# Kernel optimization log

Measured on AMD Instinct MI355X. Metric: run time of the kernel, lower is better.

## Reference

```python
import jax, jax.numpy as jnp
import numpy as np

B, H, W, CP, CI = 2, 256, 256, 256, 256
IN, OUT = CP + CI, CP          # in_dims=512, out_dims=256
WS, NH, L = 8, 8, 2            # window, heads, num blocks
N = WS * WS                    # tokens per window
HD = OUT // NH                 # head dim = 32
SCALE = HD ** -0.5

def _rel_pos_index():
    c = np.stack(np.meshgrid(np.arange(WS), np.arange(WS), indexing='ij')).reshape(2, -1)
    r = (c[:, :, None] - c[:, None, :]).transpose(1, 2, 0)
    r[..., 0] += WS - 1
    r[..., 1] += WS - 1
    r[..., 0] *= 2 * WS - 1
    return r.sum(-1)  # [N, N] int

REL_IDX = _rel_pos_index()

def _attn_mask(shift):
    img = np.zeros((H, W))
    cnt = 0
    for hs in (slice(0, -WS), slice(-WS, -shift), slice(-shift, None)):
        for ws_ in (slice(0, -WS), slice(-WS, -shift), slice(-shift, None)):
            img[hs, ws_] = cnt
            cnt += 1
    m = img.reshape(H // WS, WS, W // WS, WS).transpose(0, 2, 1, 3).reshape(-1, N)
    d = m[:, None, :] - m[:, :, None]
    return jnp.asarray(np.where(d != 0, -100.0, 0.0).astype(np.float32))  # [nW, N, N]

MASK = _attn_mask(WS // 2)

def _ln(x, g, b, eps=1e-5):
    m = x.mean(-1, keepdims=True)
    v = ((x - m) ** 2).mean(-1, keepdims=True)
    return (x - m) * jax.lax.rsqrt(v + eps) * g + b

def _win_attn(x, qkv_w, qkv_b, rpb_t, proj_w, proj_b, shift):
    # x: [B,H,W,C]
    if shift > 0:
        x = jnp.roll(x, (-shift, -shift), axis=(1, 2))
    nW = (H // WS) * (W // WS)
    xw = x.reshape(B, H // WS, WS, W // WS, WS, OUT).transpose(0, 1, 3, 2, 4, 5).reshape(B, nW, N, OUT)
    qkv = (xw @ qkv_w.T + qkv_b).reshape(B, nW, N, 3, NH, HD)
    q, k, v = qkv[..., 0, :, :], qkv[..., 1, :, :], qkv[..., 2, :, :]  # [B,nW,N,NH,HD]
    attn = jnp.einsum('bwqhd,bwkhd->bwhqk', q * SCALE, k)  # [B,nW,NH,N,N]
    bias = rpb_t[REL_IDX.reshape(-1)].reshape(N, N, NH).transpose(2, 0, 1)  # [NH,N,N]
    attn = attn + bias
    if shift > 0:
        attn = attn + MASK[None, :, None, :, :]
    attn = jax.nn.softmax(attn, axis=-1)
    out = jnp.einsum('bwhqk,bwkhd->bwqhd', attn, v).reshape(B, nW, N, OUT)
    out = out @ proj_w.T + proj_b
    out = out.reshape(B, H // WS, W // WS, WS, WS, OUT).transpose(0, 1, 3, 2, 4, 5).reshape(B, H, W, OUT)
    if shift > 0:
        out = jnp.roll(out, (shift, shift), axis=(1, 2))
    return out

def setup_inputs() -> dict:
    key = jax.random.key(0)
    ks = jax.random.split(key, 12)
    s = 0.02
    p = {}
    p['pcd'] = jax.random.normal(ks[0], (B, H, W, CP), jnp.float32)
    p['img'] = jax.random.normal(ks[1], (B, H, W, CI), jnp.float32)
    p['rd_w1'] = jax.random.normal(ks[2], (4 * IN, IN), jnp.float32) * s
    p['rd_b1'] = jnp.zeros((4 * IN,), jnp.float32)
    p['rd_lng'] = jnp.ones((4 * IN,), jnp.float32)
    p['rd_lnb'] = jnp.zeros((4 * IN,), jnp.float32)
    p['rd_w2'] = jax.random.normal(ks[3], (OUT, 4 * IN), jnp.float32) * s
    p['rd_b2'] = jnp.zeros((OUT,), jnp.float32)
    p['n1g'] = jnp.ones((L, OUT), jnp.float32)
    p['n1b'] = jnp.zeros((L, OUT), jnp.float32)
    p['qkv_w'] = jax.random.normal(ks[4], (L, 3 * OUT, OUT), jnp.float32) * s
    p['qkv_b'] = jnp.zeros((L, 3 * OUT), jnp.float32)
    p['rpb'] = jax.random.normal(ks[5], (L, (2 * WS - 1) ** 2, NH), jnp.float32) * s
    p['proj_w'] = jax.random.normal(ks[6], (L, OUT, OUT), jnp.float32) * s
    p['proj_b'] = jnp.zeros((L, OUT), jnp.float32)
    p['n2g'] = jnp.ones((L, OUT), jnp.float32)
    p['n2b'] = jnp.zeros((L, OUT), jnp.float32)
    p['mlp_w1'] = jax.random.normal(ks[7], (L, 4 * OUT, OUT), jnp.float32) * s
    p['mlp_b1'] = jnp.zeros((L, 4 * OUT), jnp.float32)
    p['mlp_w2'] = jax.random.normal(ks[8], (L, OUT, 4 * OUT), jnp.float32) * s
    p['mlp_b2'] = jnp.zeros((L, OUT), jnp.float32)
    return p

def reference(pcd, img, rd_w1, rd_b1, rd_lng, rd_lnb, rd_w2, rd_b2,
              n1g, n1b, qkv_w, qkv_b, rpb, proj_w, proj_b,
              n2g, n2b, mlp_w1, mlp_b1, mlp_w2, mlp_b2):
    # reduce_dim: Linear -> LeakyReLU(0.01) -> LayerNorm -> Linear
    x = jnp.concatenate([pcd, img], axis=3)
    x = x @ rd_w1.T + rd_b1
    x = jnp.where(x > 0, x, 0.01 * x)
    x = _ln(x, rd_lng, rd_lnb)
    x = x @ rd_w2.T + rd_b2
    # two SwinTransformerBlocks (shift 0, then WS//2)
    for i in range(L):
        shift = 0 if i % 2 == 0 else WS // 2
        x = x + _win_attn(_ln(x, n1g[i], n1b[i]), qkv_w[i], qkv_b[i], rpb[i], proj_w[i], proj_b[i], shift)
        h = _ln(x, n2g[i], n2b[i])
        h = jax.nn.gelu(h @ mlp_w1[i].T + mlp_b1[i], approximate=False)
        x = x + h @ mlp_w2[i].T + mlp_b2[i]
    return x + pcd
```

## Files before the change

kernel.cpp:

```cpp
#include <hip/hip_runtime.h>
#include <math.h>

typedef __attribute__((ext_vector_type(4))) float f32x4v;
typedef __attribute__((ext_vector_type(8))) __bf16 bf16x8v;
typedef __attribute__((ext_vector_type(2))) uint u32x2v;
typedef __attribute__((ext_vector_type(4))) uint u32x4v;

#define SCALE 0.17677669529663687f
#define TOK 131072
#define MCHUNK 32768
#define T32 ((long)TOK * 32)
#define C32 ((long)MCHUNK * 32)

__device__ __forceinline__ ushort f2bf(float v){
  const __bf16 b = (__bf16)v;
  return __builtin_bit_cast(ushort, b);
}
__device__ __forceinline__ float bflo(uint u){ return __uint_as_float(u << 16); }
__device__ __forceinline__ float bfhi(uint u){ return __uint_as_float(u & 0xffff0000u); }
__device__ __forceinline__ float bf2f(ushort u){ return __uint_as_float((uint)u << 16); }

__global__ __launch_bounds__(256) void cvtw_k(const float* __restrict__ src,
    ushort* __restrict__ dst, int K, long m32, int n4){
  const int i = blockIdx.x * 256 + threadIdx.x;
  if (i >= n4) return;
  const int flat = i * 4;
  const int r = flat / K, k = flat % K;
  float4 v = ((const float4*)src)[i];
  ushort4 o = { f2bf(v.x), f2bf(v.y), f2bf(v.z), f2bf(v.w) };
  *(ushort4*)(dst + (long)(k >> 5) * m32 + (long)r * 32 + (k & 31)) = o;
}

__global__ __launch_bounds__(64) void cvtwg_k(const float* __restrict__ src,
    const float* __restrict__ gma, const float* __restrict__ bta,
    ushort* __restrict__ dst, float* __restrict__ c1, float* __restrict__ c2,
    int K, long m32){
  const int n = blockIdx.x, lane = threadIdx.x;
  const float* sp = src + (long)n * K;
  float s1 = 0.f, s2 = 0.f;
  for (int k = lane * 4; k < K; k += 256){
    float4 wv = *(const float4*)(sp + k);
    float4 gv = *(const float4*)(gma + k);
    float4 bv = *(const float4*)(bta + k);
    s1 += wv.x * gv.x + wv.y * gv.y + wv.z * gv.z + wv.w * gv.w;
    s2 += wv.x * bv.x + wv.y * bv.y + wv.z * bv.z + wv.w * bv.w;
    ushort4 o = { f2bf(wv.x * gv.x), f2bf(wv.y * gv.y), f2bf(wv.z * gv.z), f2bf(wv.w * gv.w) };
    *(ushort4*)(dst + (long)(k >> 5) * m32 + (long)n * 32 + (k & 31)) = o;
  }
  #pragma unroll
  for (int o = 1; o < 64; o <<= 1){ s1 += __shfl_xor(s1, o); s2 += __shfl_xor(s2, o); }
  if (lane == 0){ c1[n] = s1; c2[n] = s2; }
}

__global__ __launch_bounds__(256) void concat_k(const float* __restrict__ pcd,
    const float* __restrict__ img, ushort* __restrict__ A0){
  const long gid = (long)blockIdx.x * 256 + threadIdx.x;
  const long t = gid >> 7;
  const int c4 = (int)(gid & 127) * 4;
  const float* src = (c4 < 256) ? (pcd + t * 256 + c4) : (img + t * 256 + (c4 - 256));
  float4 v = *(const float4*)src;
  ushort4 o = { f2bf(v.x), f2bf(v.y), f2bf(v.z), f2bf(v.w) };
  const long chunk = t >> 15, tc = t & 32767;
  ushort* dst = A0 + chunk * 16777216 + (long)(c4 >> 5) * C32 + tc * 32 + (c4 & 31);
  __builtin_nontemporal_store(*(u32x2v*)&o, (u32x2v*)dst);
}

__global__ __launch_bounds__(256) void statsred_k(const float* __restrict__ pb,
    float* __restrict__ stats){
  const int row = blockIdx.x * 256 + threadIdx.x;
  const float2* p = (const float2*)(pb + (long)row * 64);
  float s = 0.f, q = 0.f;
  #pragma unroll
  for (int i = 0; i < 32; ++i){ const float2 v = p[i]; s += v.x; q += v.y; }
  const float mean = s * (1.f / 2048.f);
  const float var = q * (1.f / 2048.f) - mean * mean;
  stats[row * 2] = mean;
  stats[row * 2 + 1] = rsqrtf(var + 1e-5f);
}

__global__ __launch_bounds__(256) void stats256b_k(const ushort* __restrict__ xb,
    float* __restrict__ stats){
  const int lane = threadIdx.x & 63, wd = threadIdx.x >> 6;
  const long row = (long)blockIdx.x * 4 + wd;
  uint2 u = *(const uint2*)(xb + (long)(lane >> 3) * T32 + row * 32 + (lane & 7) * 4);
  float a = bflo(u.x), b2 = bfhi(u.x), c = bflo(u.y), d = bfhi(u.y);
  float s = a + b2 + c + d;
  float q = a * a + b2 * b2 + c * c + d * d;
  #pragma unroll
  for (int o = 1; o < 64; o <<= 1){ s += __shfl_xor(s, o); q += __shfl_xor(q, o); }
  if (lane == 0){
    float mean = s * (1.f / 256.f);
    float var = q * (1.f / 256.f) - mean * mean;
    stats[row * 2] = mean;
    stats[row * 2 + 1] = rsqrtf(var + 1e-5f);
  }
}

template<int ACT, int OUTT, int RES, bool LNEPI, int MINB>
__global__ __launch_bounds__(256, MINB) void gemm_k(
    const ushort* __restrict__ A, const ushort* __restrict__ W,
    const float* __restrict__ bias,
    float* __restrict__ outf, ushort* __restrict__ outb,
    const ushort* __restrict__ res, const float* __restrict__ pcdp,
    const float* __restrict__ stats, const float* __restrict__ c1v,
    const float* __restrict__ c2v, int N, int K, int gx,
    long aM32, long wM32, long oM32, int mOff, float* __restrict__ ost)
{
  __shared__ ushort SH[16384];
  const int tid = threadIdx.x;
  const int lane = tid & 63, w = tid >> 6;
  const int nwg = gridDim.x;
  const int xcd = blockIdx.x & 7;
  const int idx = blockIdx.x >> 3;
  const int mPerX = nwg / (8 * gx);
  const int sg = idx / (8 * gx);
  const int u  = idx - sg * (8 * gx);
  const int nT = u >> 3;
  const int ml = u & 7;
  const int mBase = (xcd * mPerX + sg * 8 + ml) * 128;
  const int nBase = nT * 128;
  const int fr = lane & 15, grp = lane >> 4;
  const int wr = w >> 1, wc = w & 1;

  f32x4v acc[4][4];
  #pragma unroll
  for (int i = 0; i < 4; ++i)
    #pragma unroll
    for (int j = 0; j < 4; ++j) acc[i][j] = (f32x4v){0.f, 0.f, 0.f, 0.f};

  const long aBase = (long)(mBase + w * 32) * 32 + lane * 8;
  const long wBase = (long)(nBase + w * 32) * 32 + lane * 8;
  ushort* Ad0 = &SH[w * 1024 + lane * 8];
  ushort* Bd0 = &SH[4096 + w * 1024 + lane * 8];
  ushort* Ad1 = &SH[8192 + w * 1024 + lane * 8];
  ushort* Bd1 = &SH[12288 + w * 1024 + lane * 8];

  const int NT = K >> 5;

#define MFMASTEP(ao, bo) do { \
    bf16x8v af[4], bv[4]; \
    _Pragma("unroll") \
    for (int i = 0; i < 4; ++i) \
      af[i] = *(const bf16x8v*)&SH[(ao) + (wr * 64 + i * 16 + fr) * 32 + grp * 8]; \
    _Pragma("unroll") \
    for (int j = 0; j < 4; ++j) \
      bv[j] = *(const bf16x8v*)&SH[(bo) + (wc * 64 + j * 16 + fr) * 32 + grp * 8]; \
    _Pragma("unroll") \
    for (int i = 0; i < 4; ++i) \
      _Pragma("unroll") \
      for (int j = 0; j < 4; ++j) \
        acc[i][j] = __builtin_amdgcn_mfma_f32_16x16x32_bf16(af[i], bv[j], acc[i][j], 0, 0, 0); \
  } while (0)

  {
    uint4 x0 = *(const uint4*)(A + aBase);
    uint4 x1 = *(const uint4*)(A + aBase + 512);
    uint4 y0 = *(const uint4*)(W + wBase);
    uint4 y1 = *(const uint4*)(W + wBase + 512);
    *(uint4*)Ad0 = x0; *(uint4*)(Ad0 + 512) = x1;
    *(uint4*)Bd0 = y0; *(uint4*)(Bd0 + 512) = y1;
  }
  uint4 pa0 = *(const uint4*)(A + aBase + aM32);
  uint4 pa1 = *(const uint4*)(A + aBase + aM32 + 512);
  uint4 pb0 = *(const uint4*)(W + wBase + wM32);
  uint4 pb1 = *(const uint4*)(W + wBase + wM32 + 512);
  uint4 qa0 = *(const uint4*)(A + aBase + 2 * aM32);
  uint4 qa1 = *(const uint4*)(A + aBase + 2 * aM32 + 512);
  uint4 qb0 = *(const uint4*)(W + wBase + 2 * wM32);
  uint4 qb1 = *(const uint4*)(W + wBase + 2 * wM32 + 512);
  __syncthreads();

  for (int t = 0; t < NT; t += 2){
    MFMASTEP(0, 4096);
    *(uint4*)Ad1 = pa0; *(uint4*)(Ad1 + 512) = pa1;
    *(uint4*)Bd1 = pb0; *(uint4*)(Bd1 + 512) = pb1;
    if (t + 3 < NT){
      const long ao = aBase + (long)(t + 3) * aM32;
      const long wo = wBase + (long)(t + 3) * wM32;
      pa0 = *(const uint4*)(A + ao);
      pa1 = *(const uint4*)(A + ao + 512);
      pb0 = *(const uint4*)(W + wo);
      pb1 = *(const uint4*)(W + wo + 512);
    }
    __syncthreads();
    MFMASTEP(8192, 12288);
    if (t + 2 < NT){
      *(uint4*)Ad0 = qa0; *(uint4*)(Ad0 + 512) = qa1;
      *(uint4*)Bd0 = qb0; *(uint4*)(Bd0 + 512) = qb1;
      if (t + 4 < NT){
        const long ao = aBase + (long)(t + 4) * aM32;
        const long wo = wBase + (long)(t + 4) * wM32;
        qa0 = *(const uint4*)(A + ao);
        qa1 = *(const uint4*)(A + ao + 512);
        qb0 = *(const uint4*)(W + wo);
        qb1 = *(const uint4*)(W + wo + 512);
      }
    }
    __syncthreads();
  }
#undef MFMASTEP

  float muv[16], rsv[16];
  if (LNEPI){
    #pragma unroll
    for (int i = 0; i < 4; ++i)
      #pragma unroll
      for (int rr = 0; rr < 4; ++rr){
        const int m = mBase + wr * 64 + i * 16 + grp * 4 + rr;
        muv[i * 4 + rr] = stats[m * 2];
        rsv[i * 4 + rr] = stats[m * 2 + 1];
      }
  }
  float rsum[16], rsq[16];
  if (ost){
    #pragma unroll
    for (int t2 = 0; t2 < 16; ++t2){ rsum[t2] = 0.f; rsq[t2] = 0.f; }
  }
  #pragma unroll
  for (int j = 0; j < 4; ++j){
    const int n = nBase + wc * 64 + j * 16 + fr;
    const float bn = bias[n];
    float c1n = 0.f, c2n = 0.f;
    if (LNEPI){ c1n = c1v[n]; c2n = c2v[n]; }
    #pragma unroll
    for (int i = 0; i < 4; ++i){
      #pragma unroll
      for (int rr = 0; rr < 4; ++rr){
        const long m = mBase + wr * 64 + i * 16 + grp * 4 + rr;
        float v = acc[i][j][rr];
        if (LNEPI) v = rsv[i * 4 + rr] * v - muv[i * 4 + rr] * rsv[i * 4 + rr] * c1n + c2n;
        v += bn;
        if (ACT == 1) v = v > 0.f ? v : 0.01f * v;
        if (ACT == 2){
          const float u2 = v * (0.7978845608f + 0.0356774081f * v * v);
          const float t2 = 1.f - 2.f * __builtin_amdgcn_rcpf(__expf(2.f * u2) + 1.f);
          v = 0.5f * v * (1.f + t2);
        }
        if (RES >= 1)
          v += bf2f(res[(long)(n >> 5) * T32 + (mOff + m) * 32 + (n & 31)]);
        if (RES == 2) v += pcdp[(mOff + m) * N + n];
        acc[i][j][rr] = v;
        if (ost){ rsum[i * 4 + rr] += v; rsq[i * 4 + rr] += v * v; }
        if (OUTT == 0) __builtin_nontemporal_store(v, &outf[(mOff + m) * N + n]);
      }
    }
  }
  if (ost){
    const int nT4 = nT * 4 + wc * 2;
    #pragma unroll
    for (int t2 = 0; t2 < 16; ++t2){
      float s = rsum[t2], q = rsq[t2];
      #pragma unroll
      for (int o = 1; o < 16; o <<= 1){ s += __shfl_xor(s, o); q += __shfl_xor(q, o); }
      if (fr == 0){
        const long m = mBase + wr * 64 + (t2 >> 2) * 16 + grp * 4 + (t2 & 3);
        ost[m * 64 + nT4]     = s;
        ost[m * 64 + nT4 + 1] = q;
      }
    }
  }
  if (OUTT == 1){
    ushort* eb = &SH[0];
    __syncthreads();
    #pragma unroll
    for (int p = 0; p < 2; ++p){
      if (wr == p){
        #pragma unroll
        for (int i = 0; i < 4; ++i)
          #pragma unroll
          for (int rr = 0; rr < 4; ++rr){
            const int rl = i * 16 + grp * 4 + rr;
            #pragma unroll
            for (int j = 0; j < 4; ++j)
              eb[rl * 128 + wc * 64 + j * 16 + fr] = f2bf(acc[i][j][rr]);
          }
      }
      __syncthreads();
      #pragma unroll
      for (int it = 0; it < 4; ++it){
        const int c = it * 256 + tid;
        const int row = c >> 4, cg = c & 15;
        const u32x4v val = *(const u32x4v*)&eb[row * 128 + cg * 8];
        ushort* dst = outb + (long)((nBase >> 5) + (cg >> 2)) * oM32
                    + (long)(mOff + mBase + p * 64 + row) * 32 + (cg & 3) * 8;
        __builtin_nontemporal_store(val, (u32x4v*)dst);
      }
      __syncthreads();
    }
  }
}

template<int SHIFT>
__global__ __launch_bounds__(256, 2) void attn_k(const ushort* __restrict__ qkv,
    const float* __restrict__ rpb, ushort* __restrict__ outp)
{
  __shared__ ushort Vt[4][2312];
  __shared__ ushort Pl[4][4616];
  __shared__ float bias_s[4][226];
  __shared__ int code_s[64];
  const int tid = threadIdx.x;
  const int lane = tid & 63, wid = tid >> 6;
  const int hg = blockIdx.x & 1;
  const int bw = blockIdx.x >> 1;
  const int b = bw >> 10, widx = bw & 1023;
  const int wh = widx >> 5, ww = widx & 31;
  const int head = hg * 4 + wid;
  const int fr = lane & 15, grp = lane >> 4;

  for (int i = lane; i < 225; i += 64) bias_s[wid][i] = rpb[i * 8 + head];
  if (SHIFT > 0 && tid < 64){
    const int hh = wh * 8 + (tid >> 3), wwp = ww * 8 + (tid & 7);
    const int rh = (hh < 248) ? 0 : ((hh < 256 - SHIFT) ? 1 : 2);
    const int rw = (wwp < 248) ? 0 : ((wwp < 256 - SHIFT) ? 1 : 2);
    code_s[tid] = rh * 3 + rw;
  }
  #pragma unroll
  for (int it = 0; it < 4; ++it){
    const int c = it * 256 + tid;
    const int row = c >> 4, part = c & 15;
    const int hc = part >> 2, dc = part & 3;
    const int hs = (wh * 8 + (row >> 3) + SHIFT) & 255;
    const int wsm = (ww * 8 + (row & 7) + SHIFT) & 255;
    const long tk = ((long)b * 256 + hs) * 256 + wsm;
    const uint4 vu = *(const uint4*)(qkv + (long)(16 + hg * 4 + hc) * T32 + tk * 32 + dc * 8);
    const ushort* ve = (const ushort*)&vu;
    #pragma unroll
    for (int e = 0; e < 8; ++e)
      Vt[hc][(dc * 8 + e) * 72 + row] = ve[e];
  }
  long tokr[4];
  #pragma unroll
  for (int j = 0; j < 4; ++j){
    const int n = j * 16 + fr;
    const int hs = (wh * 8 + (n >> 3) + SHIFT) & 255;
    const int wsm = (ww * 8 + (n & 7) + SHIFT) & 255;
    tokr[j] = ((long)b * 256 + hs) * 256 + wsm;
  }
  bf16x8v kf[4];
  #pragma unroll
  for (int j = 0; j < 4; ++j)
    kf[j] = *(const bf16x8v*)(qkv + (long)(8 + head) * T32 + tokr[j] * 32 + grp * 8);
  __syncthreads();

  float invs[4][4];
  #pragma unroll
  for (int qi = 0; qi < 4; ++qi){
    const bf16x8v qf = *(const bf16x8v*)(qkv + (long)head * T32 + tokr[qi] * 32 + grp * 8);
    f32x4v sc[4];
    #pragma unroll
    for (int ci = 0; ci < 4; ++ci)
      sc[ci] = __builtin_amdgcn_mfma_f32_16x16x32_bf16(qf, kf[ci],
          (f32x4v){0.f, 0.f, 0.f, 0.f}, 0, 0, 0);
    #pragma unroll
    for (int rr = 0; rr < 4; ++rr){
      const int q = qi * 16 + grp * 4 + rr;
      const int thq = q >> 3, twq = q & 7;
      int codeq = 0;
      if (SHIFT > 0){
        const int hq = wh * 8 + thq, wq = ww * 8 + twq;
        const int rh = (hq < 248) ? 0 : ((hq < 256 - SHIFT) ? 1 : 2);
        const int rw = (wq < 248) ? 0 : ((wq < 256 - SHIFT) ? 1 : 2);
        codeq = rh * 3 + rw;
      }
      const int lbase = (thq + 7 - (fr >> 3)) * 15 + (twq + 7 - (fr & 7));
      float sum = 0.f;
      #pragma unroll
      for (int ci = 0; ci < 4; ++ci){
        float s = sc[ci][rr] * SCALE + bias_s[wid][lbase - ci * 30];
        if (SHIFT > 0 && codeq != code_s[ci * 16 + fr]) s -= 100.f;
        const float p = __expf(s);
        sum += p;
        Pl[wid][q * 72 + ci * 16 + fr] = f2bf(p);
      }
      sum += __shfl_xor(sum, 1);
      sum += __shfl_xor(sum, 2);
      sum += __shfl_xor(sum, 4);
      sum += __shfl_xor(sum, 8);
      invs[qi][rr] = __builtin_amdgcn_rcpf(sum);
    }
  }
  f32x4v o[4][2];
  #pragma unroll
  for (int qi = 0; qi < 4; ++qi)
    #pragma unroll
    for (int di = 0; di < 2; ++di) o[qi][di] = (f32x4v){0.f, 0.f, 0.f, 0.f};
  #pragma unroll
  for (int ks = 0; ks < 2; ++ks){
    bf16x8v pa[4], bvv[2];
    #pragma unroll
    for (int qi = 0; qi < 4; ++qi)
      pa[qi] = *(const bf16x8v*)&Pl[wid][(qi * 16 + fr) * 72 + ks * 32 + grp * 8];
    #pragma unroll
    for (int di = 0; di < 2; ++di)
      bvv[di] = *(const bf16x8v*)&Vt[wid][(di * 16 + fr) * 72 + ks * 32 + grp * 8];
    #pragma unroll
    for (int qi = 0; qi < 4; ++qi)
      #pragma unroll
      for (int di = 0; di < 2; ++di)
        o[qi][di] = __builtin_amdgcn_mfma_f32_16x16x32_bf16(pa[qi], bvv[di], o[qi][di], 0, 0, 0);
  }
  #pragma unroll
  for (int qi = 0; qi < 4; ++qi)
    #pragma unroll
    for (int di = 0; di < 2; ++di)
      #pragma unroll
      for (int rr = 0; rr < 4; ++rr)
        Pl[wid][(qi * 16 + grp * 4 + rr) * 72 + di * 16 + fr] =
            f2bf(o[qi][di][rr] * invs[qi][rr]);
  {
    const int n = lane;
    const int hs = (wh * 8 + (n >> 3) + SHIFT) & 255;
    const int wsm = (ww * 8 + (n & 7) + SHIFT) & 255;
    const long tokL = ((long)b * 256 + hs) * 256 + wsm;
    ushort* ob = outp + (long)head * T32 + tokL * 32;
    #pragma unroll
    for (int c4 = 0; c4 < 4; ++c4)
      *(uint4*)(ob + c4 * 8) = *(const uint4*)&Pl[wid][n * 72 + c4 * 8];
  }
}

extern "C" void kernel_launch(void* const* d_in, const int* in_sizes, int n_in,
                              void* d_out, int out_size, void* d_ws, size_t ws_size,
                              hipStream_t stream){
  const float* pcd    = (const float*)d_in[0];
  const float* img    = (const float*)d_in[1];
  const float* rd_w1  = (const float*)d_in[2];
  const float* rd_b1  = (const float*)d_in[3];
  const float* rd_lng = (const float*)d_in[4];
  const float* rd_lnb = (const float*)d_in[5];
  const float* rd_w2  = (const float*)d_in[6];
  const float* rd_b2  = (const float*)d_in[7];
  const float* n1g    = (const float*)d_in[8];
  const float* n1b    = (const float*)d_in[9];
  const float* qkv_w  = (const float*)d_in[10];
  const float* qkv_b  = (const float*)d_in[11];
  const float* rpb    = (const float*)d_in[12];
  const float* proj_w = (const float*)d_in[13];
  const float* proj_b = (const float*)d_in[14];
  const float* n2g    = (const float*)d_in[15];
  const float* n2b    = (const float*)d_in[16];
  const float* mlp_w1 = (const float*)d_in[17];
  const float* mlp_b1 = (const float*)d_in[18];
  const float* mlp_w2 = (const float*)d_in[19];
  const float* mlp_b2 = (const float*)d_in[20];

  char* ws = (char*)d_ws;
  ushort* w1b    = (ushort*)(ws + 0);
  ushort* w2g    = (ushort*)(ws + 2097152);
  ushort* qkvwg  = (ushort*)(ws + 3145728);
  ushort* projwb = (ushort*)(ws + 3932160);
  ushort* mlp1wg = (ushort*)(ws + 4194304);
  ushort* mlp2wb = (ushort*)(ws + 5242880);
  float*  cvec   = (float*)(ws + 6291456);
  float*  w2c1   = cvec,        *w2c2   = cvec + 256;
  float*  qkvc1  = cvec + 512,  *qkvc2  = cvec + 2048;
  float*  mlp1c1 = cvec + 3584, *mlp1c2 = cvec + 5632;
  float*  stats  = (float*)(ws + 6324224);
  ushort* xr     = (ushort*)(ws + 7372800);
  char*   big    = ws + 74481664;
  ushort* A0     = (ushort*)big;
  ushort* X1c    = (ushort*)(big + 134217728);
  ushort* qkvb   = (ushort*)big;
  ushort* attno  = (ushort*)(big + 201326592);
  ushort* hidden = (ushort*)big;
  float* xout = (float*)d_out;
  float* pstat = (float*)d_out;

  cvtw_k<<<1024, 256, 0, stream>>>(rd_w1, w1b, 512, 65536, 262144);
  cvtwg_k<<<256, 64, 0, stream>>>(rd_w2, rd_lng, rd_lnb, w2g, w2c1, w2c2, 2048, 8192);
  for (int i = 0; i < 2; ++i){
    cvtw_k<<<64,  256, 0, stream>>>(proj_w + i * 65536, projwb + i * 65536, 256, 8192, 16384);
    cvtw_k<<<256, 256, 0, stream>>>(mlp_w2 + i * 262144, mlp2wb + i * 262144, 1024, 8192, 65536);
    cvtwg_k<<<768, 64, 0, stream>>>(qkv_w + i * 196608, n1g + i * 256, n1b + i * 256,
        qkvwg + i * 196608, qkvc1 + i * 768, qkvc2 + i * 768, 256, 24576);
    cvtwg_k<<<1024, 64, 0, stream>>>(mlp_w1 + i * 262144, n2g + i * 256, n2b + i * 256,
        mlp1wg + i * 262144, mlp1c1 + i * 1024, mlp1c2 + i * 1024, 256, 32768);
  }
  concat_k<<<65536, 256, 0, stream>>>(pcd, img, A0);

  for (int c = 0; c < 4; ++c){
    const long off = (long)c * MCHUNK;
    gemm_k<1,1,0,false,2><<<4096, 256, 0, stream>>>(A0 + (long)c * 16777216, w1b, rd_b1,
        nullptr, X1c, nullptr, nullptr, nullptr, nullptr, nullptr,
        2048, 512, 16, C32, 65536, C32, 0, pstat);
    statsred_k<<<128, 256, 0, stream>>>(pstat, stats + off * 2);
    gemm_k<0,1,0,true,2><<<512, 256, 0, stream>>>(X1c, w2g, rd_b2,
        nullptr, xr, nullptr, nullptr,
        stats + off * 2, w2c1, w2c2,
        256, 2048, 2, C32, 8192, T32, (int)off, nullptr);
  }
  stats256b_k<<<TOK / 4, 256, 0, stream>>>(xr, stats);

  for (int i = 0; i < 2; ++i){
    gemm_k<0,1,0,true,2><<<6144, 256, 0, stream>>>(xr, qkvwg + i * 196608, qkv_b + i * 768,
        nullptr, qkvb, nullptr, nullptr, stats, qkvc1 + i * 768, qkvc2 + i * 768,
        768, 256, 6, T32, 24576, T32, 0, nullptr);
    if (i == 0)
      attn_k<0><<<4096, 256, 0, stream>>>(qkvb, rpb, attno);
    else
      attn_k<4><<<4096, 256, 0, stream>>>(qkvb, rpb + 1800, attno);
    gemm_k<0,1,1,false,2><<<2048, 256, 0, stream>>>(attno, projwb + i * 65536,
        proj_b + i * 256, nullptr, xr, xr, nullptr, nullptr, nullptr, nullptr,
        256, 256, 2, T32, 8192, T32, 0, nullptr);
    stats256b_k<<<TOK / 4, 256, 0, stream>>>(xr, stats);
    gemm_k<2,1,0,true,2><<<8192, 256, 0, stream>>>(xr, mlp1wg + i * 262144,
        mlp_b1 + i * 1024, nullptr, hidden, nullptr, nullptr,
        stats, mlp1c1 + i * 1024, mlp1c2 + i * 1024,
        1024, 256, 8, T32, 32768, T32, 0, nullptr);
    if (i == 0){
      gemm_k<0,1,1,false,2><<<2048, 256, 0, stream>>>(hidden, mlp2wb, mlp_b2,
          nullptr, xr, xr, nullptr, nullptr, nullptr, nullptr,
          256, 1024, 2, T32, 8192, T32, 0, nullptr);
      stats256b_k<<<TOK / 4, 256, 0, stream>>>(xr, stats);
    } else {
      gemm_k<0,0,2,false,2><<<2048, 256, 0, stream>>>(hidden, mlp2wb + 262144,
          mlp_b2 + 256, xout, nullptr, xr, pcd, nullptr, nullptr, nullptr,
          256, 1024, 2, T32, 8192, T32, 0, nullptr);
    }
  }
}
```

Baseline: 1.741 ms.

## Compute reduce-dim first GEMM transposed with weights as the M operand

```diff
diff --git a/kernel.cpp b/kernel.cpp
--- a/kernel.cpp
+++ b/kernel.cpp
@@ -96,7 +96,7 @@
   }
 }
 
-template<int ACT, int OUTT, int RES, bool LNEPI, int MINB>
+template<int ACT, int OUTT, int RES, bool LNEPI, int MINB, bool TRB>
 __global__ __launch_bounds__(256, MINB) void gemm_k(
     const ushort* __restrict__ A, const ushort* __restrict__ W,
     const float* __restrict__ bias,
@@ -106,19 +106,24 @@
     const float* __restrict__ c2v, int N, int K, int gx,
     long aM32, long wM32, long oM32, int mOff, float* __restrict__ ost)
 {
-  __shared__ ushort SH[16384];
+  __shared__ ushort SH[17408];
   const int tid = threadIdx.x;
   const int lane = tid & 63, w = tid >> 6;
   const int nwg = gridDim.x;
   const int xcd = blockIdx.x & 7;
   const int idx = blockIdx.x >> 3;
-  const int mPerX = nwg / (8 * gx);
-  const int sg = idx / (8 * gx);
-  const int u  = idx - sg * (8 * gx);
-  const int nT = u >> 3;
-  const int ml = u & 7;
-  const int mBase = (xcd * mPerX + sg * 8 + ml) * 128;
-  const int nBase = nT * 128;
+  int mBase, nBase;
+  if (TRB){
+    const int npx = nwg / (8 * gx);
+    mBase = (idx % gx) * 128;
+    nBase = (xcd * npx + idx / gx) * 128;
+  } else {
+    const int mPerX = nwg / (8 * gx);
+    const int sg = idx / (8 * gx);
+    const int u  = idx - sg * (8 * gx);
+    mBase = ((xcd * mPerX + sg * 8 + (u & 7))) * 128;
+    nBase = (u >> 3) * 128;
+  }
   const int fr = lane & 15, grp = lane >> 4;
   const int wr = w >> 1, wc = w & 1;
 
@@ -200,6 +205,63 @@
   }
 #undef MFMASTEP
 
+  if (TRB){
+    float bm[16];
+    #pragma unroll
+    for (int i = 0; i < 4; ++i)
+      #pragma unroll
+      for (int rr = 0; rr < 4; ++rr)
+        bm[i * 4 + rr] = bias[mBase + wr * 64 + i * 16 + grp * 4 + rr];
+    float csum[4], csq[4];
+    #pragma unroll
+    for (int j = 0; j < 4; ++j){ csum[j] = 0.f; csq[j] = 0.f; }
+    #pragma unroll
+    for (int j = 0; j < 4; ++j){
+      #pragma unroll
+      for (int i = 0; i < 4; ++i){
+        #pragma unroll
+        for (int rr = 0; rr < 4; ++rr){
+          float v = acc[i][j][rr] + bm[i * 4 + rr];
+          v = v > 0.f ? v : 0.01f * v;
+          acc[i][j][rr] = v;
+          csum[j] += v; csq[j] += v * v;
+        }
+      }
+    }
+    const int mT = mBase >> 7;
+    #pragma unroll
+    for (int j = 0; j < 4; ++j){
+      float s = csum[j], q = csq[j];
+      s += __shfl_xor(s, 16); q += __shfl_xor(q, 16);
+      s += __shfl_xor(s, 32); q += __shfl_xor(q, 32);
+      if (lane < 16){
+        const long ntok = nBase + wc * 64 + j * 16 + lane;
+        ost[ntok * 64 + mT * 4 + wr * 2]     = s;
+        ost[ntok * 64 + mT * 4 + wr * 2 + 1] = q;
+      }
+    }
+    ushort* eb = &SH[0];
+    __syncthreads();
+    #pragma unroll
+    for (int j = 0; j < 4; ++j){
+      const int ncol = wc * 64 + j * 16 + fr;
+      #pragma unroll
+      for (int i = 0; i < 4; ++i)
+        #pragma unroll
+        for (int rr = 0; rr < 4; ++rr)
+          eb[ncol * 136 + wr * 64 + i * 16 + grp * 4 + rr] = f2bf(acc[i][j][rr]);
+    }
+    __syncthreads();
+    #pragma unroll
+    for (int it = 0; it < 8; ++it){
+      const int c = it * 256 + tid;
+      const int trow = c >> 4, cg = c & 15;
+      const u32x4v val = *(const u32x4v*)&eb[trow * 136 + cg * 8];
+      ushort* dst = outb + (long)((mBase >> 5) + (cg >> 2)) * oM32
+                  + (long)(nBase + trow) * 32 + (cg & 3) * 8;
+      __builtin_nontemporal_store(val, (u32x4v*)dst);
+    }
+  } else {
   float muv[16], rsv[16];
   if (LNEPI){
     #pragma unroll
@@ -246,7 +308,7 @@
     }
   }
   if (ost){
-    const int nT4 = nT * 4 + wc * 2;
+    const int nT4 = (nBase >> 7) * 4 + wc * 2;
     #pragma unroll
     for (int t2 = 0; t2 < 16; ++t2){
       float s = rsum[t2], q = rsq[t2];
@@ -281,12 +343,13 @@
         const int c = it * 256 + tid;
         const int row = c >> 4, cg = c & 15;
         const u32x4v val = *(const u32x4v*)&eb[row * 128 + cg * 8];
-        ushort* dst = outb + (long)((nBase >> 5) + (cg >> 2)) * oM32
+        ushort* dst = outb + (long)(((nBase) >> 5) + (cg >> 2)) * oM32
                     + (long)(mOff + mBase + p * 64 + row) * 32 + (cg & 3) * 8;
         __builtin_nontemporal_store(val, (u32x4v*)dst);
       }
       __syncthreads();
     }
+  }
   }
 }
 
@@ -480,11 +543,11 @@
 
   for (int c = 0; c < 4; ++c){
     const long off = (long)c * MCHUNK;
-    gemm_k<1,1,0,false,2><<<4096, 256, 0, stream>>>(A0 + (long)c * 16777216, w1b, rd_b1,
-        nullptr, X1c, nullptr, nullptr, nullptr, nullptr, nullptr,
-        2048, 512, 16, C32, 65536, C32, 0, pstat);
+    gemm_k<1,1,0,false,2,true><<<4096, 256, 0, stream>>>(w1b, A0 + (long)c * 16777216,
+        rd_b1, nullptr, X1c, nullptr, nullptr, nullptr, nullptr, nullptr,
+        32768, 512, 16, 65536, C32, C32, 0, pstat);
     statsred_k<<<128, 256, 0, stream>>>(pstat, stats + off * 2);
-    gemm_k<0,1,0,true,2><<<512, 256, 0, stream>>>(X1c, w2g, rd_b2,
+    gemm_k<0,1,0,true,2,false><<<512, 256, 0, stream>>>(X1c, w2g, rd_b2,
         nullptr, xr, nullptr, nullptr,
         stats + off * 2, w2c1, w2c2,
         256, 2048, 2, C32, 8192, T32, (int)off, nullptr);
@@ -492,28 +555,28 @@
   stats256b_k<<<TOK / 4, 256, 0, stream>>>(xr, stats);
 
   for (int i = 0; i < 2; ++i){
-    gemm_k<0,1,0,true,2><<<6144, 256, 0, stream>>>(xr, qkvwg + i * 196608, qkv_b + i * 768,
-        nullptr, qkvb, nullptr, nullptr, stats, qkvc1 + i * 768, qkvc2 + i * 768,
-        768, 256, 6, T32, 24576, T32, 0, nullptr);
+    gemm_k<0,1,0,true,2,false><<<6144, 256, 0, stream>>>(xr, qkvwg + i * 196608,
+        qkv_b + i * 768, nullptr, qkvb, nullptr, nullptr, stats,
+        qkvc1 + i * 768, qkvc2 + i * 768, 768, 256, 6, T32, 24576, T32, 0, nullptr);
     if (i == 0)
       attn_k<0><<<4096, 256, 0, stream>>>(qkvb, rpb, attno);
     else
       attn_k<4><<<4096, 256, 0, stream>>>(qkvb, rpb + 1800, attno);
-    gemm_k<0,1,1,false,2><<<2048, 256, 0, stream>>>(attno, projwb + i * 65536,
+    gemm_k<0,1,1,false,2,false><<<2048, 256, 0, stream>>>(attno, projwb + i * 65536,
         proj_b + i * 256, nullptr, xr, xr, nullptr, nullptr, nullptr, nullptr,
         256, 256, 2, T32, 8192, T32, 0, nullptr);
     stats256b_k<<<TOK / 4, 256, 0, stream>>>(xr, stats);
-    gemm_k<2,1,0,true,2><<<8192, 256, 0, stream>>>(xr, mlp1wg + i * 262144,
+    gemm_k<2,1,0,true,2,false><<<8192, 256, 0, stream>>>(xr, mlp1wg + i * 262144,
         mlp_b1 + i * 1024, nullptr, hidden, nullptr, nullptr,
         stats, mlp1c1 + i * 1024, mlp1c2 + i * 1024,
         1024, 256, 8, T32, 32768, T32, 0, nullptr);
     if (i == 0){
-      gemm_k<0,1,1,false,2><<<2048, 256, 0, stream>>>(hidden, mlp2wb, mlp_b2,
+      gemm_k<0,1,1,false,2,false><<<2048, 256, 0, stream>>>(hidden, mlp2wb, mlp_b2,
           nullptr, xr, xr, nullptr, nullptr, nullptr, nullptr,
           256, 1024, 2, T32, 8192, T32, 0, nullptr);
       stats256b_k<<<TOK / 4, 256, 0, stream>>>(xr, stats);
     } else {
-      gemm_k<0,0,2,false,2><<<2048, 256, 0, stream>>>(hidden, mlp2wb + 262144,
+      gemm_k<0,0,2,false,2,false><<<2048, 256, 0, stream>>>(hidden, mlp2wb + 262144,
           mlp_b2 + 256, xout, nullptr, xr, pcd, nullptr, nullptr, nullptr,
           256, 1024, 2, T32, 8192, T32, 0, nullptr);
     }
```

Measured after the change: 1.722 ms, median of 3. Within noise of the previous version (-1.1%).
